# Kernel tuning notes

Hardware: AMD Instinct MI355X
Metric: run time of the kernel (lower is better)

## Reference

```python
import jax, jax.numpy as jnp
import numpy as np

# hyperparams (from init_kwargs / opt)
POS_W, NEG_W = 2.0, 40.0
MARGIN, THRESH = 0.1, 0.5
TAU, ALPHA, BETA = 4.0, 1.0, 0.5
N_EPOCHS = 100
F_STANDARD = False
N_CLASSES = 100


def setup_inputs() -> dict:
    key = jax.random.key(0)
    k1, k2, k3 = jax.random.split(key, 3)
    B, D = 4096, 128
    batch = jax.random.normal(k1, (B, D), dtype=jnp.float32)
    batch = batch / jnp.linalg.norm(batch, axis=1, keepdims=True)
    teacher = jax.random.normal(k2, (B, D), dtype=jnp.float32)
    teacher = teacher / jnp.linalg.norm(teacher, axis=1, keepdims=True)
    labels = jax.random.randint(k3, (B,), 0, N_CLASSES, dtype=jnp.int64 if jax.config.jax_enable_x64 else jnp.int32)
    return {"batch": batch, "teacher_batch": teacher, "labels": labels, "epoch": 50}


def reference(batch, teacher_batch, labels, epoch):
    B = batch.shape[0]
    sim = batch @ batch.T                              # [B,B]
    same = labels[:, None] == labels[None, :]          # [B,B]
    eye = jnp.eye(B, dtype=bool)
    pos = same & ~eye
    neg = ~same

    inf = jnp.float32(jnp.inf)
    min_pos = jnp.min(jnp.where(pos, sim, inf), axis=1)    # [B]
    max_neg = jnp.max(jnp.where(neg, sim, -inf), axis=1)   # [B]
    neg_keep = neg & (sim + MARGIN > min_pos[:, None])
    pos_keep = pos & (sim - MARGIN < max_neg[:, None])
    valid = jnp.any(neg_keep, axis=1) & jnp.any(pos_keep, axis=1)

    # masked log-sum-exp terms; exp(-inf)=0 keeps masked entries (and grads) zero
    pos_term = (1.0 / POS_W) * jnp.log1p(
        jnp.sum(jnp.exp(jnp.where(pos_keep, -POS_W * (sim - THRESH), -inf)), axis=1))
    neg_term = (1.0 / NEG_W) * jnp.log1p(
        jnp.sum(jnp.exp(jnp.where(neg_keep, NEG_W * (sim - THRESH), -inf)), axis=1))
    n_valid = jnp.maximum(jnp.sum(valid.astype(sim.dtype)), 1.0)
    loss_rank = jnp.sum(jnp.where(valid, pos_term + neg_term, 0.0)) / n_valid

    # KD term: per-anchor concat(pos_sims, neg_sims) is a permutation of the full
    # row, and softmax/KL are permutation invariant -> apply per-element scaling.
    t_sim = teacher_batch @ teacher_batch.T
    scale = jnp.ones_like(sim) if F_STANDARD else jnp.where(neg, BETA, 1.0)
    log_p = jax.nn.log_softmax(sim * scale / TAU, axis=1)
    q = jax.lax.stop_gradient(jax.nn.softmax(t_sim * scale / TAU, axis=1))
    # KLDivLoss(batchmean) on a [1,B] row == sum(q * (log q - log_p))
    kl_rows = jnp.sum(q * (jnp.log(q) - log_p), axis=1)   # [B]
    loss_kd = jnp.mean(kl_rows)

    loss = loss_rank + (epoch / N_EPOCHS) * ALPHA * (TAU ** 2) * loss_kd
    return (loss, loss_rank, loss_kd)
```

## Files before the change

### kernel.cpp

```cpp
#include <hip/hip_runtime.h>
#include <hip/hip_fp16.h>
#include <math.h>

#define BB  4096
#define DD  128
#define NCH 16
#define NP  8
#define TB  256

typedef __attribute__((ext_vector_type(8))) _Float16 half8;
typedef __attribute__((ext_vector_type(4))) float f32x4;

constexpr float POS_W  = 2.0f;
constexpr float NEG_W  = 40.0f;
constexpr float MARGIN = 0.1f;
constexpr float THRESH = 0.5f;

__device__ __forceinline__ unsigned short f2h(float f) {
  __half h = __float2half(f);
  return __half_as_ushort(h);
}
__device__ __forceinline__ f32x4 mfma16h(half8 a, half8 b, f32x4 c) {
  return __builtin_amdgcn_mfma_f32_16x16x32_f16(a, b, c, 0, 0, 0);
}
__device__ __forceinline__ void gll16(const void* g, void* l) {
  __builtin_amdgcn_global_load_lds(
      (const __attribute__((address_space(1))) void*)g,
      (__attribute__((address_space(3))) void*)l, 16, 0, 0);
}

__global__ __launch_bounds__(256) void k0(
    const float* __restrict__ b, const float* __restrict__ t,
    unsigned short* __restrict__ xf, unsigned short* __restrict__ yf,
    int* __restrict__ cnt)
{
  const int i = blockIdx.x * 256 + threadIdx.x;
  if (i == 0) *cnt = 0;
  {
    float4 v = reinterpret_cast<const float4*>(b)[i];
    ushort4 h;
    h.x = f2h(v.x); h.y = f2h(v.y); h.z = f2h(v.z); h.w = f2h(v.w);
    reinterpret_cast<ushort4*>(xf)[i] = h;
  }
  {
    float4 v = reinterpret_cast<const float4*>(t)[i];
    ushort4 h;
    h.x = f2h(v.x); h.y = f2h(v.y); h.z = f2h(v.z); h.w = f2h(v.w);
    reinterpret_cast<ushort4*>(yf)[i] = h;
  }
}


__global__ __launch_bounds__(TB, 2) void kG1(
    const unsigned short* __restrict__ xf, const unsigned short* __restrict__ yf,
    const int* __restrict__ labels,
    float* __restrict__ zsP, float* __restrict__ mpP, float* __restrict__ mnP,
    float* __restrict__ ztP, float* __restrict__ wvP)
{
  __shared__ unsigned short sB[2][8192];
  __shared__ int sJlab[256];

  const int tid  = threadIdx.x;
  const int lane = tid & 63;
  const int wid  = tid >> 6;
  const int ag   = blockIdx.x & 31;
  const int ch   = blockIdx.x >> 5;
  const int i0w  = ag * 128 + wid * 32;
  const int l15  = lane & 15;
  const int hi_l = lane >> 4;
  const int rbase = hi_l * 4;
  const int koff  = hi_l * 8;
  const int j0ch  = ch * 256;
  const int srow  = lane & 31;
  const int sk0   = wid * 32 + (lane >> 5) * 8;

  sJlab[tid] = labels[j0ch + tid];

  half8 Ax[2][4], Ay[2][4];
#pragma unroll
  for (int at = 0; at < 2; ++at) {
    const size_t ab = (size_t)(i0w + at * 16 + l15) * DD + koff;
#pragma unroll
    for (int s = 0; s < 4; ++s) {
      Ax[at][s] = *reinterpret_cast<const half8*>(xf + ab + s * 32);
      Ay[at][s] = *reinterpret_cast<const half8*>(yf + ab + s * 32);
    }
  }
  int labA[2][4];
#pragma unroll
  for (int at = 0; at < 2; ++at)
#pragma unroll
    for (int r = 0; r < 4; ++r) labA[at][r] = labels[i0w + at * 16 + rbase + r];

  float zs[2][4], mp[2][4], mn[2][4], zt[2][4], wv[2][4];
#pragma unroll
  for (int at = 0; at < 2; ++at)
#pragma unroll
    for (int r = 0; r < 4; ++r) {
      zs[at][r] = 0.f; mp[at][r] = INFINITY; mn[at][r] = -INFINITY;
      zt[at][r] = 0.f; wv[at][r] = 0.f;
    }

  {
    const size_t g0 = (size_t)(j0ch + srow) * DD + sk0;
    gll16(xf + g0,      &sB[0][wid * 1024]);
    gll16(xf + g0 + 16, &sB[0][wid * 1024 + 512]);
    gll16(yf + g0,      &sB[0][4096 + wid * 1024]);
    gll16(yf + g0 + 16, &sB[0][4096 + wid * 1024 + 512]);
  }

#pragma unroll 1
  for (int pp = 0; pp < NP; ++pp) {
    const int cur = pp & 1;
    __syncthreads();
    if (pp + 1 < NP) {
      const size_t g0 = (size_t)(j0ch + (pp + 1) * 32 + srow) * DD + sk0;
      gll16(xf + g0,      &sB[cur ^ 1][wid * 1024]);
      gll16(xf + g0 + 16, &sB[cur ^ 1][wid * 1024 + 512]);
      gll16(yf + g0,      &sB[cur ^ 1][4096 + wid * 1024]);
      gll16(yf + g0 + 16, &sB[cur ^ 1][4096 + wid * 1024 + 512]);
    }

    f32x4 aS[2][2], aT[2][2];
#pragma unroll
    for (int at = 0; at < 2; ++at)
#pragma unroll
      for (int t = 0; t < 2; ++t) { aS[at][t] = {0.f,0.f,0.f,0.f}; aT[at][t] = {0.f,0.f,0.f,0.f}; }
#pragma unroll
    for (int s = 0; s < 4; ++s) {
#pragma unroll
      for (int t = 0; t < 2; ++t) {
        const int ro = (s * 128 + hi_l * 32 + t * 16 + l15) * 8;
        half8 vX = *reinterpret_cast<const half8*>(&sB[cur][ro]);
        half8 vY = *reinterpret_cast<const half8*>(&sB[cur][4096 + ro]);
        aS[0][t] = mfma16h(Ax[0][s], vX, aS[0][t]);
        aS[1][t] = mfma16h(Ax[1][s], vX, aS[1][t]);
        aT[0][t] = mfma16h(Ay[0][s], vY, aT[0][t]);
        aT[1][t] = mfma16h(Ay[1][s], vY, aT[1][t]);
      }
    }

#pragma unroll
    for (int t = 0; t < 2; ++t) {
      const int lj   = sJlab[pp * 32 + t * 16 + l15];
      const int jcol = j0ch + pp * 32 + t * 16 + l15;
#pragma unroll
      for (int at = 0; at < 2; ++at)
#pragma unroll
        for (int r = 0; r < 4; ++r) {
          float sim = aS[at][t][r], tsim = aT[at][t][r];
          bool same = (lj == labA[at][r]);
          float sc = same ? 0.25f : 0.125f;
          float s  = sim * sc;
          float ts = tsim * sc;
          zs[at][r] += __expf(s);
          float et = __expf(ts);
          zt[at][r] += et;
          wv[at][r] += et * (ts - s);
          if (same) {
            if (jcol != i0w + at * 16 + rbase + r) mp[at][r] = fminf(mp[at][r], sim);
          } else {
            mn[at][r] = fmaxf(mn[at][r], sim);
          }
        }
    }
  }

#pragma unroll
  for (int at = 0; at < 2; ++at)
#pragma unroll
    for (int r = 0; r < 4; ++r)
#pragma unroll
      for (int m = 1; m < 16; m <<= 1) {
        zs[at][r] += __shfl_xor(zs[at][r], m);
        mp[at][r] = fminf(mp[at][r], __shfl_xor(mp[at][r], m));
        mn[at][r] = fmaxf(mn[at][r], __shfl_xor(mn[at][r], m));
        zt[at][r] += __shfl_xor(zt[at][r], m);
        wv[at][r] += __shfl_xor(wv[at][r], m);
      }
  if (l15 == 0) {
#pragma unroll
    for (int at = 0; at < 2; ++at)
#pragma unroll
      for (int r = 0; r < 4; ++r) {
        const int i_r = i0w + at * 16 + rbase + r;
        zsP[ch * BB + i_r] = zs[at][r];
        mpP[ch * BB + i_r] = mp[at][r];
        mnP[ch * BB + i_r] = mn[at][r];
        ztP[ch * BB + i_r] = zt[at][r];
        wvP[ch * BB + i_r] = wv[at][r];
      }
  }
}

__global__ __launch_bounds__(TB, 3) void kG2(
    const unsigned short* __restrict__ xf,
    const int* __restrict__ labels,
    const float* __restrict__ mpP, const float* __restrict__ mnP,
    float* __restrict__ psP, float* __restrict__ nsP)
{
  __shared__ unsigned short sX[2][4096];
  __shared__ int sJlab[256];
  __shared__ float sMPr[128], sMNr[128];

  const int tid  = threadIdx.x;
  const int lane = tid & 63;
  const int wid  = tid >> 6;
  const int ag   = blockIdx.x & 31;
  const int ch   = blockIdx.x >> 5;
  const int i0w  = ag * 128 + wid * 32;
  const int l15  = lane & 15;
  const int hi_l = lane >> 4;
  const int rbase = hi_l * 4;
  const int koff  = hi_l * 8;
  const int j0ch  = ch * 256;
  const int srow  = lane & 31;
  const int sk0   = wid * 32 + (lane >> 5) * 8;

  {
    const size_t g0 = (size_t)(j0ch + srow) * DD + sk0;
    gll16(xf + g0,      &sX[0][wid * 1024]);
    gll16(xf + g0 + 16, &sX[0][wid * 1024 + 512]);
  }

  sJlab[tid] = labels[j0ch + tid];
  if (tid < 128) {
    const int aidx = ag * 128 + tid;
    float a = INFINITY, b = -INFINITY;
#pragma unroll
    for (int c = 0; c < NCH; ++c) {
      a = fminf(a, mpP[c * BB + aidx]);
      b = fmaxf(b, mnP[c * BB + aidx]);
    }
    sMPr[tid] = a; sMNr[tid] = b;
  }

  half8 Ax[2][4];
#pragma unroll
  for (int at = 0; at < 2; ++at) {
    const size_t ab = (size_t)(i0w + at * 16 + l15) * DD + koff;
#pragma unroll
    for (int s = 0; s < 4; ++s)
      Ax[at][s] = *reinterpret_cast<const half8*>(xf + ab + s * 32);
  }
  int labA[2][4];
#pragma unroll
  for (int at = 0; at < 2; ++at)
#pragma unroll
    for (int r = 0; r < 4; ++r) labA[at][r] = labels[i0w + at * 16 + rbase + r];

  __syncthreads();
  float mpA[2][4], mnA[2][4];
#pragma unroll
  for (int at = 0; at < 2; ++at)
#pragma unroll
    for (int r = 0; r < 4; ++r) {
      const int al = wid * 32 + at * 16 + rbase + r;
      mpA[at][r] = sMPr[al];
      mnA[at][r] = sMNr[al];
    }

  float ps[2][4], ns[2][4];
#pragma unroll
  for (int at = 0; at < 2; ++at)
#pragma unroll
    for (int r = 0; r < 4; ++r) { ps[at][r] = 0.f; ns[at][r] = 0.f; }

#pragma unroll 1
  for (int pp = 0; pp < NP; ++pp) {
    const int cur = pp & 1;
    __syncthreads();
    if (pp + 1 < NP) {
      const size_t g0 = (size_t)(j0ch + (pp + 1) * 32 + srow) * DD + sk0;
      gll16(xf + g0,      &sX[cur ^ 1][wid * 1024]);
      gll16(xf + g0 + 16, &sX[cur ^ 1][wid * 1024 + 512]);
    }

    f32x4 acc[2][2];
#pragma unroll
    for (int at = 0; at < 2; ++at)
#pragma unroll
      for (int t = 0; t < 2; ++t) acc[at][t] = {0.f, 0.f, 0.f, 0.f};
#pragma unroll
    for (int s = 0; s < 4; ++s) {
#pragma unroll
      for (int t = 0; t < 2; ++t) {
        const int ro = (s * 128 + hi_l * 32 + t * 16 + l15) * 8;
        half8 vB = *reinterpret_cast<const half8*>(&sX[cur][ro]);
        acc[0][t] = mfma16h(Ax[0][s], vB, acc[0][t]);
        acc[1][t] = mfma16h(Ax[1][s], vB, acc[1][t]);
      }
    }

#pragma unroll
    for (int t = 0; t < 2; ++t) {
      const int lj   = sJlab[pp * 32 + t * 16 + l15];
      const int jcol = j0ch + pp * 32 + t * 16 + l15;
#pragma unroll
      for (int at = 0; at < 2; ++at)
#pragma unroll
        for (int r = 0; r < 4; ++r) {
          float sim = acc[at][t][r];
          bool same = (lj == labA[at][r]);
          if (same) {
            if (jcol != i0w + at * 16 + rbase + r && (sim - MARGIN < mnA[at][r]))
              ps[at][r] += __expf(-POS_W * (sim - THRESH));
          } else {
            if (sim + MARGIN > mpA[at][r])
              ns[at][r] += __expf(NEG_W * (sim - THRESH));
          }
        }
    }
  }

#pragma unroll
  for (int at = 0; at < 2; ++at)
#pragma unroll
    for (int r = 0; r < 4; ++r)
#pragma unroll
      for (int m = 1; m < 16; m <<= 1) {
        ps[at][r] += __shfl_xor(ps[at][r], m);
        ns[at][r] += __shfl_xor(ns[at][r], m);
      }
  if (l15 == 0) {
#pragma unroll
    for (int at = 0; at < 2; ++at)
#pragma unroll
      for (int r = 0; r < 4; ++r) {
        const int i_r = i0w + at * 16 + rbase + r;
        psP[ch * BB + i_r] = ps[at][r];
        nsP[ch * BB + i_r] = ns[at][r];
      }
  }
}

__global__ __launch_bounds__(512) void kD(
    const float* __restrict__ zsP, const float* __restrict__ ztP,
    const float* __restrict__ wvP, const float* __restrict__ psP,
    const float* __restrict__ nsP, const int* __restrict__ epoch,
    double* __restrict__ rkP, double* __restrict__ kdP, int* __restrict__ nvP,
    int* __restrict__ cnt, float* __restrict__ out)
{
  __shared__ double sR[8], sK[8];
  __shared__ int    sN[8];
  const int tid = threadIdx.x;
  const int lane = tid & 63;
  const int wid = tid >> 6;
  const int i = blockIdx.x * 512 + tid;

  float zs = 0.f, zt = 0.f, wv = 0.f, ps = 0.f, ns = 0.f;
#pragma unroll
  for (int c = 0; c < NCH; ++c) {
    zs += zsP[c * BB + i];
    zt += ztP[c * BB + i];
    wv += wvP[c * BB + i];
    ps += psP[c * BB + i];
    ns += nsP[c * BB + i];
  }
  double kd = (double)(wv / zt + __logf(zs) - __logf(zt));
  double rank = 0.0; int nv = 0;
  if (ps > 0.f && ns > 0.f) {
    rank = (double)(log1pf(ps) * 0.5f + log1pf(ns) * 0.025f);
    nv = 1;
  }
#pragma unroll
  for (int o = 32; o; o >>= 1) {
    rank += __shfl_xor(rank, o);
    kd   += __shfl_xor(kd, o);
    nv   += __shfl_xor(nv, o);
  }
  if (lane == 0) { sR[wid] = rank; sK[wid] = kd; sN[wid] = nv; }
  __syncthreads();
  if (tid == 0) {
    double R_ = 0.0, K_ = 0.0; int N_ = 0;
    for (int w = 0; w < 8; ++w) { R_ += sR[w]; K_ += sK[w]; N_ += sN[w]; }
    rkP[blockIdx.x] = R_;
    kdP[blockIdx.x] = K_;
    nvP[blockIdx.x] = N_;
    __threadfence();
    int old = atomicAdd(cnt, 1);
    if (old == 7) {
      __threadfence();
      double RT = 0.0, KT = 0.0; int NT = 0;
      for (int b = 0; b < 8; ++b) { RT += rkP[b]; KT += kdP[b]; NT += nvP[b]; }
      double loss_rank = RT / (double)(NT < 1 ? 1 : NT);
      double loss_kd   = KT / (double)BB;
      double wgt = (double)epoch[0] * 0.16;
      out[0] = (float)(loss_rank + wgt * loss_kd);
      out[1] = (float)loss_rank;
      out[2] = (float)loss_kd;
      *cnt = 0;
    }
  }
}

extern "C" void kernel_launch(void* const* d_in, const int* in_sizes, int n_in,
                              void* d_out, int out_size, void* d_ws, size_t ws_size,
                              hipStream_t stream)
{
  (void)in_sizes; (void)n_in; (void)out_size; (void)ws_size;
  const float* batch   = (const float*)d_in[0];
  const float* teacher = (const float*)d_in[1];
  const int*   labels  = (const int*)d_in[2];
  const int*   epoch   = (const int*)d_in[3];
  float* out = (float*)d_out;

  char* w = (char*)d_ws;
  const size_t MB = 1048576;
  unsigned short* xf = (unsigned short*)(w + 0 * MB);
  unsigned short* yf = (unsigned short*)(w + 1 * MB);
  const size_t PCH = (size_t)NCH * BB * sizeof(float);
  float* zsP = (float*)(w + 2 * MB + 0 * PCH);
  float* mpP = (float*)(w + 2 * MB + 1 * PCH);
  float* mnP = (float*)(w + 2 * MB + 2 * PCH);
  float* ztP = (float*)(w + 2 * MB + 3 * PCH);
  float* wvP = (float*)(w + 2 * MB + 4 * PCH);
  float* psP = (float*)(w + 2 * MB + 5 * PCH);
  float* nsP = (float*)(w + 2 * MB + 6 * PCH);
  double* rkP = (double*)(w + 4 * MB);
  double* kdP = (double*)(w + 4 * MB + 64);
  int*    nvP = (int*)(w + 4 * MB + 128);
  int*    cnt = (int*)(w + 4 * MB + 192);

  k0<<<dim3(BB * DD / 4 / 256), dim3(256), 0, stream>>>(batch, teacher, xf, yf, cnt);
  kG1<<<dim3(32 * NCH), dim3(TB), 0, stream>>>(xf, yf, labels,
                                               zsP, mpP, mnP, ztP, wvP);
  kG2<<<dim3(32 * NCH), dim3(TB), 0, stream>>>(xf, labels, mpP, mnP, psP, nsP);
  kD<<<dim3(8), dim3(512), 0, stream>>>(zsP, ztP, wvP, psP, nsP, epoch,
                                        rkP, kdP, nvP, cnt, out);
}
```

Baseline: 59.30 us.

## Fuse all four kernels into one cooperative persistent kernel with grid syncs

Replaces the four-launch pipeline (convert, similarity stats, rank sums, final reduce) with a single cooperative kernel of 256 blocks. It separates the phases with grid.sync instead of kernel boundaries, and each block loops over two column chunks. This removes launch gaps and inter-kernel drain. The cost is half the previous grid parallelism (256 blocks at one block per CU versus 512 blocks at two), plus grid-barrier overhead. It falls back to the old launches if the cooperative launch fails, and also drops one redundant barrier in kG2.

```diff
diff --git a/kernel.cpp b/kernel.cpp
--- a/kernel.cpp
+++ b/kernel.cpp
@@ -1,12 +1,16 @@
 #include <hip/hip_runtime.h>
 #include <hip/hip_fp16.h>
+#include <hip/hip_cooperative_groups.h>
 #include <math.h>
+
+namespace cg = cooperative_groups;
 
 #define BB  4096
 #define DD  128
 #define NCH 16
 #define NP  8
 #define TB  256
+#define CGRID 256
 
 typedef __attribute__((ext_vector_type(8))) _Float16 half8;
 typedef __attribute__((ext_vector_type(4))) float f32x4;
@@ -27,6 +31,361 @@
   __builtin_amdgcn_global_load_lds(
       (const __attribute__((address_space(1))) void*)g,
       (__attribute__((address_space(3))) void*)l, 16, 0, 0);
+}
+
+
+__global__ __launch_bounds__(TB, 1) void fused(
+    const float* __restrict__ batch, const float* __restrict__ teacher,
+    const int* __restrict__ labels, const int* __restrict__ epoch,
+    unsigned short* __restrict__ xf, unsigned short* __restrict__ yf,
+    float* __restrict__ zsP, float* __restrict__ mpP, float* __restrict__ mnP,
+    float* __restrict__ ztP, float* __restrict__ wvP,
+    float* __restrict__ psP, float* __restrict__ nsP,
+    double* __restrict__ rkP, double* __restrict__ kdP, int* __restrict__ nvP,
+    int* __restrict__ cnt, float* __restrict__ out)
+{
+  __shared__ unsigned short sMem[16384];
+  __shared__ int   sJlab[256];
+  __shared__ float sRed[256];
+  __shared__ double sDr[4], sDk[4];
+  __shared__ int    sNn[4];
+
+  cg::grid_group grid = cg::this_grid();
+
+  const int tid  = threadIdx.x;
+  const int lane = tid & 63;
+  const int wid  = tid >> 6;
+  const int bid  = blockIdx.x;
+
+  {
+    if (bid == 0 && tid == 0) *cnt = 0;
+#pragma unroll
+    for (int it = 0; it < 2; ++it) {
+      const int i = it * (CGRID * TB) + bid * TB + tid;
+      {
+        float4 v = reinterpret_cast<const float4*>(batch)[i];
+        ushort4 h;
+        h.x = f2h(v.x); h.y = f2h(v.y); h.z = f2h(v.z); h.w = f2h(v.w);
+        reinterpret_cast<ushort4*>(xf)[i] = h;
+      }
+      {
+        float4 v = reinterpret_cast<const float4*>(teacher)[i];
+        ushort4 h;
+        h.x = f2h(v.x); h.y = f2h(v.y); h.z = f2h(v.z); h.w = f2h(v.w);
+        reinterpret_cast<ushort4*>(yf)[i] = h;
+      }
+    }
+  }
+  grid.sync();
+
+  const int ag   = bid & 31;
+  const int ch0  = bid >> 5;
+  const int i0w  = ag * 128 + wid * 32;
+  const int l15  = lane & 15;
+  const int hi_l = lane >> 4;
+  const int rbase = hi_l * 4;
+  const int koff  = hi_l * 8;
+  const int srow  = lane & 31;
+  const int sk0   = wid * 32 + (lane >> 5) * 8;
+
+  int labA[2][4];
+#pragma unroll
+  for (int at = 0; at < 2; ++at)
+#pragma unroll
+    for (int r = 0; r < 4; ++r) labA[at][r] = labels[i0w + at * 16 + rbase + r];
+
+  {
+    half8 Ax[2][4], Ay[2][4];
+#pragma unroll
+    for (int at = 0; at < 2; ++at) {
+      const size_t ab = (size_t)(i0w + at * 16 + l15) * DD + koff;
+#pragma unroll
+      for (int s = 0; s < 4; ++s) {
+        Ax[at][s] = *reinterpret_cast<const half8*>(xf + ab + s * 32);
+        Ay[at][s] = *reinterpret_cast<const half8*>(yf + ab + s * 32);
+      }
+    }
+
+#pragma unroll 1
+    for (int cc = ch0; cc < NCH; cc += 8) {
+      const int j0ch = cc * 256;
+      __syncthreads();
+      sJlab[tid] = labels[j0ch + tid];
+
+      float zs[2][4], mp[2][4], mn[2][4], zt[2][4], wv[2][4];
+#pragma unroll
+      for (int at = 0; at < 2; ++at)
+#pragma unroll
+        for (int r = 0; r < 4; ++r) {
+          zs[at][r] = 0.f; mp[at][r] = INFINITY; mn[at][r] = -INFINITY;
+          zt[at][r] = 0.f; wv[at][r] = 0.f;
+        }
+
+      {
+        const size_t g0 = (size_t)(j0ch + srow) * DD + sk0;
+        gll16(xf + g0,      &sMem[wid * 1024]);
+        gll16(xf + g0 + 16, &sMem[wid * 1024 + 512]);
+        gll16(yf + g0,      &sMem[4096 + wid * 1024]);
+        gll16(yf + g0 + 16, &sMem[4096 + wid * 1024 + 512]);
+      }
+
+#pragma unroll 1
+      for (int pp = 0; pp < NP; ++pp) {
+        const int cur = pp & 1;
+        const int cb  = cur * 8192;
+        __syncthreads();
+        if (pp + 1 < NP) {
+          const int nb = (cur ^ 1) * 8192;
+          const size_t g0 = (size_t)(j0ch + (pp + 1) * 32 + srow) * DD + sk0;
+          gll16(xf + g0,      &sMem[nb + wid * 1024]);
+          gll16(xf + g0 + 16, &sMem[nb + wid * 1024 + 512]);
+          gll16(yf + g0,      &sMem[nb + 4096 + wid * 1024]);
+          gll16(yf + g0 + 16, &sMem[nb + 4096 + wid * 1024 + 512]);
+        }
+
+        f32x4 aS[2][2], aT[2][2];
+#pragma unroll
+        for (int at = 0; at < 2; ++at)
+#pragma unroll
+          for (int t = 0; t < 2; ++t) { aS[at][t] = {0.f,0.f,0.f,0.f}; aT[at][t] = {0.f,0.f,0.f,0.f}; }
+#pragma unroll
+        for (int s = 0; s < 4; ++s) {
+#pragma unroll
+          for (int t = 0; t < 2; ++t) {
+            const int ro = (s * 128 + hi_l * 32 + t * 16 + l15) * 8;
+            half8 vX = *reinterpret_cast<const half8*>(&sMem[cb + ro]);
+            half8 vY = *reinterpret_cast<const half8*>(&sMem[cb + 4096 + ro]);
+            aS[0][t] = mfma16h(Ax[0][s], vX, aS[0][t]);
+            aS[1][t] = mfma16h(Ax[1][s], vX, aS[1][t]);
+            aT[0][t] = mfma16h(Ay[0][s], vY, aT[0][t]);
+            aT[1][t] = mfma16h(Ay[1][s], vY, aT[1][t]);
+          }
+        }
+
+#pragma unroll
+        for (int t = 0; t < 2; ++t) {
+          const int lj   = sJlab[pp * 32 + t * 16 + l15];
+          const int jcol = j0ch + pp * 32 + t * 16 + l15;
+#pragma unroll
+          for (int at = 0; at < 2; ++at)
+#pragma unroll
+            for (int r = 0; r < 4; ++r) {
+              float sim = aS[at][t][r], tsim = aT[at][t][r];
+              bool same = (lj == labA[at][r]);
+              float sc = same ? 0.25f : 0.125f;
+              float s  = sim * sc;
+              float ts = tsim * sc;
+              zs[at][r] += __expf(s);
+              float et = __expf(ts);
+              zt[at][r] += et;
+              wv[at][r] += et * (ts - s);
+              if (same) {
+                if (jcol != i0w + at * 16 + rbase + r) mp[at][r] = fminf(mp[at][r], sim);
+              } else {
+                mn[at][r] = fmaxf(mn[at][r], sim);
+              }
+            }
+        }
+      }
+
+#pragma unroll
+      for (int at = 0; at < 2; ++at)
+#pragma unroll
+        for (int r = 0; r < 4; ++r)
+#pragma unroll
+          for (int m = 1; m < 16; m <<= 1) {
+            zs[at][r] += __shfl_xor(zs[at][r], m);
+            mp[at][r] = fminf(mp[at][r], __shfl_xor(mp[at][r], m));
+            mn[at][r] = fmaxf(mn[at][r], __shfl_xor(mn[at][r], m));
+            zt[at][r] += __shfl_xor(zt[at][r], m);
+            wv[at][r] += __shfl_xor(wv[at][r], m);
+          }
+      if (l15 == 0) {
+#pragma unroll
+        for (int at = 0; at < 2; ++at)
+#pragma unroll
+          for (int r = 0; r < 4; ++r) {
+            const int i_r = i0w + at * 16 + rbase + r;
+            zsP[cc * BB + i_r] = zs[at][r];
+            mpP[cc * BB + i_r] = mp[at][r];
+            mnP[cc * BB + i_r] = mn[at][r];
+            ztP[cc * BB + i_r] = zt[at][r];
+            wvP[cc * BB + i_r] = wv[at][r];
+          }
+      }
+    }
+  }
+  grid.sync();
+
+  {
+    half8 Ax[2][4];
+#pragma unroll
+    for (int at = 0; at < 2; ++at) {
+      const size_t ab = (size_t)(i0w + at * 16 + l15) * DD + koff;
+#pragma unroll
+      for (int s = 0; s < 4; ++s)
+        Ax[at][s] = *reinterpret_cast<const half8*>(xf + ab + s * 32);
+    }
+
+    if (tid < 128) {
+      const int aidx = ag * 128 + tid;
+      float a = INFINITY, b = -INFINITY;
+#pragma unroll
+      for (int c = 0; c < NCH; ++c) {
+        a = fminf(a, mpP[c * BB + aidx]);
+        b = fmaxf(b, mnP[c * BB + aidx]);
+      }
+      sRed[tid] = a; sRed[128 + tid] = b;
+    }
+    __syncthreads();
+    float mpA[2][4], mnA[2][4];
+#pragma unroll
+    for (int at = 0; at < 2; ++at)
+#pragma unroll
+      for (int r = 0; r < 4; ++r) {
+        const int al = wid * 32 + at * 16 + rbase + r;
+        mpA[at][r] = sRed[al];
+        mnA[at][r] = sRed[128 + al];
+      }
+
+#pragma unroll 1
+    for (int cc = ch0; cc < NCH; cc += 8) {
+      const int j0ch = cc * 256;
+      __syncthreads();
+      sJlab[tid] = labels[j0ch + tid];
+
+      {
+        const size_t g0 = (size_t)(j0ch + srow) * DD + sk0;
+        gll16(xf + g0,      &sMem[wid * 1024]);
+        gll16(xf + g0 + 16, &sMem[wid * 1024 + 512]);
+      }
+
+      float ps[2][4], ns[2][4];
+#pragma unroll
+      for (int at = 0; at < 2; ++at)
+#pragma unroll
+        for (int r = 0; r < 4; ++r) { ps[at][r] = 0.f; ns[at][r] = 0.f; }
+
+#pragma unroll 1
+      for (int pp = 0; pp < NP; ++pp) {
+        const int cur = pp & 1;
+        const int cb  = cur * 4096;
+        __syncthreads();
+        if (pp + 1 < NP) {
+          const int nb = (cur ^ 1) * 4096;
+          const size_t g0 = (size_t)(j0ch + (pp + 1) * 32 + srow) * DD + sk0;
+          gll16(xf + g0,      &sMem[nb + wid * 1024]);
+          gll16(xf + g0 + 16, &sMem[nb + wid * 1024 + 512]);
+        }
+
+        f32x4 acc[2][2];
+#pragma unroll
+        for (int at = 0; at < 2; ++at)
+#pragma unroll
+          for (int t = 0; t < 2; ++t) acc[at][t] = {0.f, 0.f, 0.f, 0.f};
+#pragma unroll
+        for (int s = 0; s < 4; ++s) {
+#pragma unroll
+          for (int t = 0; t < 2; ++t) {
+            const int ro = (s * 128 + hi_l * 32 + t * 16 + l15) * 8;
+            half8 vB = *reinterpret_cast<const half8*>(&sMem[cb + ro]);
+            acc[0][t] = mfma16h(Ax[0][s], vB, acc[0][t]);
+            acc[1][t] = mfma16h(Ax[1][s], vB, acc[1][t]);
+          }
+        }
+
+#pragma unroll
+        for (int t = 0; t < 2; ++t) {
+          const int lj   = sJlab[pp * 32 + t * 16 + l15];
+          const int jcol = j0ch + pp * 32 + t * 16 + l15;
+#pragma unroll
+          for (int at = 0; at < 2; ++at)
+#pragma unroll
+            for (int r = 0; r < 4; ++r) {
+              float sim = acc[at][t][r];
+              bool same = (lj == labA[at][r]);
+              if (same) {
+                if (jcol != i0w + at * 16 + rbase + r && (sim - MARGIN < mnA[at][r]))
+                  ps[at][r] += __expf(-POS_W * (sim - THRESH));
+              } else {
+                if (sim + MARGIN > mpA[at][r])
+                  ns[at][r] += __expf(NEG_W * (sim - THRESH));
+              }
+            }
+        }
+      }
+
+#pragma unroll
+      for (int at = 0; at < 2; ++at)
+#pragma unroll
+        for (int r = 0; r < 4; ++r)
+#pragma unroll
+          for (int m = 1; m < 16; m <<= 1) {
+            ps[at][r] += __shfl_xor(ps[at][r], m);
+            ns[at][r] += __shfl_xor(ns[at][r], m);
+          }
+      if (l15 == 0) {
+#pragma unroll
+        for (int at = 0; at < 2; ++at)
+#pragma unroll
+          for (int r = 0; r < 4; ++r) {
+            const int i_r = i0w + at * 16 + rbase + r;
+            psP[cc * BB + i_r] = ps[at][r];
+            nsP[cc * BB + i_r] = ns[at][r];
+          }
+      }
+    }
+  }
+  grid.sync();
+
+  if (bid < 16) {
+    const int i = bid * TB + tid;
+
+    float zs = 0.f, zt = 0.f, wv = 0.f, ps = 0.f, ns = 0.f;
+#pragma unroll
+    for (int c = 0; c < NCH; ++c) {
+      zs += zsP[c * BB + i];
+      zt += ztP[c * BB + i];
+      wv += wvP[c * BB + i];
+      ps += psP[c * BB + i];
+      ns += nsP[c * BB + i];
+    }
+    double kd = (double)(wv / zt + __logf(zs) - __logf(zt));
+    double rank = 0.0; int nv = 0;
+    if (ps > 0.f && ns > 0.f) {
+      rank = (double)(log1pf(ps) * 0.5f + log1pf(ns) * 0.025f);
+      nv = 1;
+    }
+#pragma unroll
+    for (int o = 32; o; o >>= 1) {
+      rank += __shfl_xor(rank, o);
+      kd   += __shfl_xor(kd, o);
+      nv   += __shfl_xor(nv, o);
+    }
+    if (lane == 0) { sDr[wid] = rank; sDk[wid] = kd; sNn[wid] = nv; }
+    __syncthreads();
+    if (tid == 0) {
+      double R_ = 0.0, K_ = 0.0; int N_ = 0;
+      for (int w2 = 0; w2 < 4; ++w2) { R_ += sDr[w2]; K_ += sDk[w2]; N_ += sNn[w2]; }
+      rkP[bid] = R_;
+      kdP[bid] = K_;
+      nvP[bid] = N_;
+      __threadfence();
+      int old = atomicAdd(cnt, 1);
+      if (old == 15) {
+        __threadfence();
+        double RT = 0.0, KT = 0.0; int NT = 0;
+        for (int b = 0; b < 16; ++b) { RT += rkP[b]; KT += kdP[b]; NT += nvP[b]; }
+        double loss_rank = RT / (double)(NT < 1 ? 1 : NT);
+        double loss_kd   = KT / (double)BB;
+        double wgt = (double)epoch[0] * 0.16;
+        out[0] = (float)(loss_rank + wgt * loss_kd);
+        out[1] = (float)loss_rank;
+        out[2] = (float)loss_kd;
+        *cnt = 0;
+      }
+    }
+  }
 }
 
 __global__ __launch_bounds__(256) void k0(
@@ -49,7 +408,6 @@
     reinterpret_cast<ushort4*>(yf)[i] = h;
   }
 }
-
 
 __global__ __launch_bounds__(TB, 2) void kG1(
     const unsigned short* __restrict__ xf, const unsigned short* __restrict__ yf,
@@ -269,7 +627,7 @@
 #pragma unroll 1
   for (int pp = 0; pp < NP; ++pp) {
     const int cur = pp & 1;
-    __syncthreads();
+    if (pp) __syncthreads();
     if (pp + 1 < NP) {
       const size_t g0 = (size_t)(j0ch + (pp + 1) * 32 + srow) * DD + sk0;
       gll16(xf + g0,      &sX[cur ^ 1][wid * 1024]);
@@ -418,14 +776,23 @@
   float* psP = (float*)(w + 2 * MB + 5 * PCH);
   float* nsP = (float*)(w + 2 * MB + 6 * PCH);
   double* rkP = (double*)(w + 4 * MB);
-  double* kdP = (double*)(w + 4 * MB + 64);
-  int*    nvP = (int*)(w + 4 * MB + 128);
-  int*    cnt = (int*)(w + 4 * MB + 192);
-
-  k0<<<dim3(BB * DD / 4 / 256), dim3(256), 0, stream>>>(batch, teacher, xf, yf, cnt);
-  kG1<<<dim3(32 * NCH), dim3(TB), 0, stream>>>(xf, yf, labels,
-                                               zsP, mpP, mnP, ztP, wvP);
-  kG2<<<dim3(32 * NCH), dim3(TB), 0, stream>>>(xf, labels, mpP, mnP, psP, nsP);
-  kD<<<dim3(8), dim3(512), 0, stream>>>(zsP, ztP, wvP, psP, nsP, epoch,
-                                        rkP, kdP, nvP, cnt, out);
-}
+  double* kdP = (double*)(w + 4 * MB + 256);
+  int*    nvP = (int*)(w + 4 * MB + 512);
+  int*    cnt = (int*)(w + 4 * MB + 640);
+
+  void* args[] = { (void*)&batch, (void*)&teacher, (void*)&labels, (void*)&epoch,
+                   (void*)&xf, (void*)&yf,
+                   (void*)&zsP, (void*)&mpP, (void*)&mnP, (void*)&ztP, (void*)&wvP,
+                   (void*)&psP, (void*)&nsP,
+                   (void*)&rkP, (void*)&kdP, (void*)&nvP, (void*)&cnt, (void*)&out };
+  hipError_t err = hipLaunchCooperativeKernel((const void*)fused, dim3(CGRID),
+                                              dim3(TB), args, 0, stream);
+  if (err != hipSuccess) {
+    k0<<<dim3(BB * DD / 4 / 256), dim3(256), 0, stream>>>(batch, teacher, xf, yf, cnt);
+    kG1<<<dim3(32 * NCH), dim3(TB), 0, stream>>>(xf, yf, labels,
+                                                 zsP, mpP, mnP, ztP, wvP);
+    kG2<<<dim3(32 * NCH), dim3(TB), 0, stream>>>(xf, labels, mpP, mnP, psP, nsP);
+    kD<<<dim3(8), dim3(512), 0, stream>>>(zsP, ztP, wvP, psP, nsP, epoch,
+                                          rkP, kdP, nvP, cnt, out);
+  }
+}
```

Measured after the change: 174.4 us. +194.2%, slower.

## Materialize fp16 similarity matrix in kG1 and reuse it in kG2

Applied to the files above, without the earlier changes.

kG1 now writes its student similarity tiles to a global workspace as fp16, in a lane-ordered layout. kG2 reads these tiles back instead of reloading the embeddings and redoing the MFMA GEMM. With the LDS buffers and A-fragment registers gone, kG2's occupancy hint goes from 3 to 4 blocks. The trade is a 32 MB write plus read of global memory against a cheap 128-deep GEMM, and sim values used in the margin tests and the exp(40·x) terms are now rounded to fp16, which may affect accuracy.

```diff
diff --git a/kernel.cpp b/kernel.cpp
--- a/kernel.cpp
+++ b/kernel.cpp
@@ -19,6 +19,11 @@
 __device__ __forceinline__ unsigned short f2h(float f) {
   __half h = __float2half(f);
   return __half_as_ushort(h);
+}
+__device__ __forceinline__ float h2f(unsigned short u) {
+  _Float16 h;
+  __builtin_memcpy(&h, &u, 2);
+  return (float)h;
 }
 __device__ __forceinline__ f32x4 mfma16h(half8 a, half8 b, f32x4 c) {
   return __builtin_amdgcn_mfma_f32_16x16x32_f16(a, b, c, 0, 0, 0);
@@ -55,7 +60,8 @@
     const unsigned short* __restrict__ xf, const unsigned short* __restrict__ yf,
     const int* __restrict__ labels,
     float* __restrict__ zsP, float* __restrict__ mpP, float* __restrict__ mnP,
-    float* __restrict__ ztP, float* __restrict__ wvP)
+    float* __restrict__ ztP, float* __restrict__ wvP,
+    ushort4* __restrict__ simh4)
 {
   __shared__ unsigned short sB[2][8192];
   __shared__ int sJlab[256];
@@ -74,6 +80,8 @@
   const int srow  = lane & 31;
   const int sk0   = wid * 32 + (lane >> 5) * 8;
 
+  ushort4* sblk = simh4 + (size_t)blockIdx.x * 8192 + wid * 2048 + lane;
+
   sJlab[tid] = labels[j0ch + tid];
 
   half8 Ax[2][4], Ay[2][4];
@@ -139,6 +147,16 @@
         aT[1][t] = mfma16h(Ay[1][s], vY, aT[1][t]);
       }
     }
+
+#pragma unroll
+    for (int t = 0; t < 2; ++t)
+#pragma unroll
+      for (int at = 0; at < 2; ++at) {
+        ushort4 h4;
+        h4.x = f2h(aS[at][t][0]); h4.y = f2h(aS[at][t][1]);
+        h4.z = f2h(aS[at][t][2]); h4.w = f2h(aS[at][t][3]);
+        sblk[((pp * 2 + t) * 2 + at) * 64] = h4;
+      }
 
 #pragma unroll
     for (int t = 0; t < 2; ++t) {
@@ -193,13 +211,12 @@
   }
 }
 
-__global__ __launch_bounds__(TB, 3) void kG2(
-    const unsigned short* __restrict__ xf,
+__global__ __launch_bounds__(TB, 4) void kG2(
+    const ushort4* __restrict__ simh4,
     const int* __restrict__ labels,
     const float* __restrict__ mpP, const float* __restrict__ mnP,
     float* __restrict__ psP, float* __restrict__ nsP)
 {
-  __shared__ unsigned short sX[2][4096];
   __shared__ int sJlab[256];
   __shared__ float sMPr[128], sMNr[128];
 
@@ -212,16 +229,7 @@
   const int l15  = lane & 15;
   const int hi_l = lane >> 4;
   const int rbase = hi_l * 4;
-  const int koff  = hi_l * 8;
   const int j0ch  = ch * 256;
-  const int srow  = lane & 31;
-  const int sk0   = wid * 32 + (lane >> 5) * 8;
-
-  {
-    const size_t g0 = (size_t)(j0ch + srow) * DD + sk0;
-    gll16(xf + g0,      &sX[0][wid * 1024]);
-    gll16(xf + g0 + 16, &sX[0][wid * 1024 + 512]);
-  }
 
   sJlab[tid] = labels[j0ch + tid];
   if (tid < 128) {
@@ -235,14 +243,6 @@
     sMPr[tid] = a; sMNr[tid] = b;
   }
 
-  half8 Ax[2][4];
-#pragma unroll
-  for (int at = 0; at < 2; ++at) {
-    const size_t ab = (size_t)(i0w + at * 16 + l15) * DD + koff;
-#pragma unroll
-    for (int s = 0; s < 4; ++s)
-      Ax[at][s] = *reinterpret_cast<const half8*>(xf + ab + s * 32);
-  }
   int labA[2][4];
 #pragma unroll
   for (int at = 0; at < 2; ++at)
@@ -266,41 +266,21 @@
 #pragma unroll
     for (int r = 0; r < 4; ++r) { ps[at][r] = 0.f; ns[at][r] = 0.f; }
 
-#pragma unroll 1
+  const ushort4* sblk = simh4 + (size_t)blockIdx.x * 8192 + wid * 2048 + lane;
+
+#pragma unroll 2
   for (int pp = 0; pp < NP; ++pp) {
-    const int cur = pp & 1;
-    __syncthreads();
-    if (pp + 1 < NP) {
-      const size_t g0 = (size_t)(j0ch + (pp + 1) * 32 + srow) * DD + sk0;
-      gll16(xf + g0,      &sX[cur ^ 1][wid * 1024]);
-      gll16(xf + g0 + 16, &sX[cur ^ 1][wid * 1024 + 512]);
-    }
-
-    f32x4 acc[2][2];
-#pragma unroll
-    for (int at = 0; at < 2; ++at)
-#pragma unroll
-      for (int t = 0; t < 2; ++t) acc[at][t] = {0.f, 0.f, 0.f, 0.f};
-#pragma unroll
-    for (int s = 0; s < 4; ++s) {
-#pragma unroll
-      for (int t = 0; t < 2; ++t) {
-        const int ro = (s * 128 + hi_l * 32 + t * 16 + l15) * 8;
-        half8 vB = *reinterpret_cast<const half8*>(&sX[cur][ro]);
-        acc[0][t] = mfma16h(Ax[0][s], vB, acc[0][t]);
-        acc[1][t] = mfma16h(Ax[1][s], vB, acc[1][t]);
-      }
-    }
-
 #pragma unroll
     for (int t = 0; t < 2; ++t) {
       const int lj   = sJlab[pp * 32 + t * 16 + l15];
       const int jcol = j0ch + pp * 32 + t * 16 + l15;
 #pragma unroll
-      for (int at = 0; at < 2; ++at)
+      for (int at = 0; at < 2; ++at) {
+        ushort4 v = sblk[((pp * 2 + t) * 2 + at) * 64];
+        float sv[4] = { h2f(v.x), h2f(v.y), h2f(v.z), h2f(v.w) };
 #pragma unroll
         for (int r = 0; r < 4; ++r) {
-          float sim = acc[at][t][r];
+          float sim = sv[r];
           bool same = (lj == labA[at][r]);
           if (same) {
             if (jcol != i0w + at * 16 + rbase + r && (sim - MARGIN < mnA[at][r]))
@@ -310,6 +290,7 @@
               ns[at][r] += __expf(NEG_W * (sim - THRESH));
           }
         }
+      }
     }
   }
 
@@ -418,14 +399,15 @@
   float* psP = (float*)(w + 2 * MB + 5 * PCH);
   float* nsP = (float*)(w + 2 * MB + 6 * PCH);
   double* rkP = (double*)(w + 4 * MB);
-  double* kdP = (double*)(w + 4 * MB + 64);
-  int*    nvP = (int*)(w + 4 * MB + 128);
-  int*    cnt = (int*)(w + 4 * MB + 192);
+  double* kdP = (double*)(w + 4 * MB + 256);
+  int*    nvP = (int*)(w + 4 * MB + 512);
+  int*    cnt = (int*)(w + 4 * MB + 640);
+  ushort4* simh4 = (ushort4*)(w + 8 * MB);
 
   k0<<<dim3(BB * DD / 4 / 256), dim3(256), 0, stream>>>(batch, teacher, xf, yf, cnt);
   kG1<<<dim3(32 * NCH), dim3(TB), 0, stream>>>(xf, yf, labels,
-                                               zsP, mpP, mnP, ztP, wvP);
-  kG2<<<dim3(32 * NCH), dim3(TB), 0, stream>>>(xf, labels, mpP, mnP, psP, nsP);
+                                               zsP, mpP, mnP, ztP, wvP, simh4);
+  kG2<<<dim3(32 * NCH), dim3(TB), 0, stream>>>(simh4, labels, mpP, mnP, psP, nsP);
   kD<<<dim3(8), dim3(512), 0, stream>>>(zsP, ztP, wvP, psP, nsP, epoch,
                                         rkP, kdP, nvP, cnt, out);
 }
```

Measured after the change: 65.09 us. +9.8%, slower.
